# Performance work log

Measured on AMD Instinct MI355X. Metric: run time of the kernel, lower is better.

Reference implementation:

```python
import jax, jax.numpy as jnp
import numpy as np

B, R, N, DN, DR, H, Q, NB = 32, 10, 512, 128, 128, 128, 256, 16


def setup_inputs() -> dict:
    key = jax.random.key(0)
    ks = jax.random.split(key, 14)
    inp = {
        'node_features': jax.random.normal(ks[0], (B, N, DN), jnp.float32),
        'relation_features': jax.random.normal(ks[1], (B, R, DR), jnp.float32),
        'adj': jax.random.uniform(ks[2], (B, R, N, N), jnp.float32),
        'obs': jax.random.normal(ks[3], (B, Q, H), jnp.float32),
        'node_mask': jnp.ones((B, N), jnp.float32),
        'obs_mask': jnp.ones((B, Q), jnp.float32),
        # RGCN params (single layer: hidden_dims=[128])
        'Wb': jax.random.normal(ks[4], (NB, (DN + DR) * R), jnp.float32) * 0.02,  # bottleneck (no bias)
        'Ww': jax.random.normal(ks[5], (H, NB), jnp.float32) * 0.1,               # weight (no bias)
        'rgcn_bias': jnp.zeros((), jnp.float32),                                   # scalar bias (filled 0)
        # ContextQueryAttention params
        'w_C': jax.random.normal(ks[6], (H,), jnp.float32) * 0.05,
        'w_Q': jax.random.normal(ks[7], (H,), jnp.float32) * 0.05,
        'w_CQ': jax.random.normal(ks[8], (H,), jnp.float32) * 0.05,
        'cq_bias': jnp.zeros((), jnp.float32),
        # ReprAggregator output linear (shared for both directions)
        'lin_W': jax.random.normal(ks[9], (H, 4 * H), jnp.float32) * 0.02,
        'lin_b': jnp.zeros((H,), jnp.float32),
    }
    return inp


def _masked_softmax(s, mask, axis):
    return jax.nn.softmax(jnp.where(mask > 0, s, -jnp.inf), axis=axis)


def _rgcn(node_features, relation_features, adj, Wb, Ww, rgcn_bias):
    b, n = node_features.shape[0], node_features.shape[1]
    # per-relation concat: (B,R,N,DN+DR)
    nf = jnp.broadcast_to(node_features[:, None], (b, R, n, node_features.shape[-1]))
    rf = jnp.broadcast_to(relation_features[:, :, None, :], (b, R, n, relation_features.shape[-1]))
    cat = jnp.concatenate([nf, rf], axis=-1)
    # per-relation bmm, gathered in relation order along feature dim: (B,N,R*(DN+DR))
    sup = jnp.einsum('brnm,brmd->bnrd', adj, cat)
    sup = sup.reshape(b, n, R * cat.shape[-1])
    h = sup @ Wb.T            # (B,N,NB)
    h = h @ Ww.T              # (B,N,H)
    return jax.nn.sigmoid(h + rgcn_bias)


def _cqattn(ctx, query, ctx_mask, query_mask, w_C, w_Q, w_CQ, cq_bias):
    # trilinear similarity: (B,Lc,Lq)
    res_C = ctx @ w_C                                  # (B,Lc)
    res_Q = query @ w_Q                                # (B,Lq)
    res_CQ = jnp.einsum('bch,bqh->bcq', ctx * w_CQ, query)
    S = res_C[:, :, None] + res_Q[:, None, :] + res_CQ + cq_bias
    s_ctx = _masked_softmax(S, ctx_mask[:, :, None], axis=1)     # softmax over ctx dim
    s_query = _masked_softmax(S, query_mask[:, None, :], axis=2)  # softmax over query dim
    P = jnp.einsum('bcq,bqh->bch', s_query, query)
    Qm = jnp.einsum('bcq,bdq,bdh->bch', s_query, s_ctx, ctx)
    return jnp.concatenate([ctx, P, ctx * P, ctx * Qm], axis=-1)  # (B,Lc,4H)


def reference(node_features, relation_features, adj, obs, node_mask, obs_mask,
              Wb, Ww, rgcn_bias, w_C, w_Q, w_CQ, cq_bias, lin_W, lin_b):
    # GraphEncoder (single RGCN layer)
    node_repr = _rgcn(node_features, relation_features, adj, Wb, Ww, rgcn_bias)
    # ReprAggregator between obs text repr and node repr
    a1 = _cqattn(obs, node_repr, obs_mask, node_mask, w_C, w_Q, w_CQ, cq_bias)
    a2 = _cqattn(node_repr, obs, node_mask, obs_mask, w_C, w_Q, w_CQ, cq_bias)
    h_og = a1 @ lin_W.T + lin_b   # (B,Q,H)
    h_go = a2 @ lin_W.T + lin_b   # (B,N,H)
    return h_og, h_go
```

## Files before the change

### kernel.cpp

```cpp
#include <hip/hip_runtime.h>
#include <hip/hip_bf16.h>
#include <stdint.h>

typedef unsigned short u16;
typedef __attribute__((ext_vector_type(8))) short short8;
typedef __attribute__((ext_vector_type(4))) float f32x4;

#define DEVI static __device__ __forceinline__

constexpr int B = 32, R = 10, N = 512, H = 128, Q = 256, NB = 16;
constexpr int KWB = 2560;

DEVI u16 f2u(float f) { return __builtin_bit_cast(unsigned short, __float2bfloat16(f)); }
DEVI float u2f(u16 u) { union { uint32_t i; float f; } c; c.i = ((uint32_t)u) << 16; return c.f; }

DEVI float wredmax(float v) { for (int o = 32; o; o >>= 1) v = fmaxf(v, __shfl_xor(v, o)); return v; }
DEVI float wredsum(float v) { for (int o = 32; o; o >>= 1) v += __shfl_xor(v, o); return v; }

DEVI short8 cvt8(const float* p) {
  float4 f0 = *(const float4*)p;
  float4 f1 = *(const float4*)(p + 4);
  short8 v;
  v[0] = (short)f2u(f0.x); v[1] = (short)f2u(f0.y);
  v[2] = (short)f2u(f0.z); v[3] = (short)f2u(f0.w);
  v[4] = (short)f2u(f1.x); v[5] = (short)f2u(f1.y);
  v[6] = (short)f2u(f1.z); v[7] = (short)f2u(f1.w);
  return v;
}

__global__ __launch_bounds__(256) void k_prep(
    const float* __restrict__ linW, u16* __restrict__ linWb,
    const float* __restrict__ Wb, u16* __restrict__ WbB,
    const float* __restrict__ Ww, u16* __restrict__ WwB,
    const float* __restrict__ rf, float* __restrict__ vv,
    const float* __restrict__ obs, const float* __restrict__ wC,
    const float* __restrict__ wQ, const float* __restrict__ wCQ,
    u16* __restrict__ obsW, float* __restrict__ a_o, float* __restrict__ d_o,
    u16* __restrict__ obsT) {
  int bid = blockIdx.x, t = threadIdx.x;
  __shared__ float sa[4], sd[4];
  __shared__ u16 tile[32][33];
  if (bid < 64) {
    int i = bid * 256 + t;
    float4 f = ((const float4*)linW)[i];
    ushort4 o;
    o.x = f2u(f.x); o.y = f2u(f.y); o.z = f2u(f.z); o.w = f2u(f.w);
    ((ushort4*)linWb)[i] = o;
  } else if (bid < 144) {
    int rk = (bid - 64) * 2 + (t >> 7);
    int d = t & 127;
    int r = rk / NB, k = rk % NB;
    WbB[(long)rk * 128 + d] = f2u(Wb[(long)k * KWB + r * 256 + d]);
  } else if (bid < 160) {
    int idx = (bid - 144) * 256 + t;
    int h = idx >> 5, kb = idx & 31;
    WwB[idx] = (kb < NB) ? f2u(Ww[h * NB + kb]) : (u16)0;
  } else if (bid < 1440) {
    int w = t >> 6, lane = t & 63;
    int gid = (bid - 160) * 4 + w;
    int b = gid / (R * NB), rk = gid % (R * NB), r = rk / NB, k = rk % NB;
    float s = 0.f;
    for (int dd = 0; dd < 2; ++dd) {
      int d = lane + dd * 64;
      s += rf[((long)b * R + r) * H + d] * Wb[(long)k * KWB + r * 256 + 128 + d];
    }
    s = wredsum(s);
    if (lane == 0) vv[((long)b * R + r) * NB + k] = s;
  } else if (bid < 5536) {
    int row = (bid - 1440) * 2 + (t >> 7);
    int tt = t & 127;
    float x = obs[(long)row * H + tt];
    obsW[(long)row * H + tt] = f2u(x * wCQ[tt]);
    float aa = wredsum(x * wC[tt]);
    float dd2 = wredsum(x * wQ[tt]);
    int wv = t >> 6;
    if ((t & 63) == 0) { sa[wv] = aa; sd[wv] = dd2; }
    __syncthreads();
    if ((t & 127) == 0) {
      int h = t >> 7;
      a_o[row] = sa[h * 2] + sa[h * 2 + 1];
      d_o[row] = sd[h * 2] + sd[h * 2 + 1];
    }
  } else {
    int id = bid - 5536;
    int cx = id & 3, ry = (id >> 2) & 7, b = id >> 5;
    int c0 = cx * 32, r0 = ry * 32;
    int tx = t & 31, ty = t >> 5;
    for (int i = 0; i < 4; i++) {
      int r = r0 + ty + i * 8, c = c0 + tx;
      tile[ty + i * 8][tx] = f2u(obs[((long)b * Q + r) * H + c]);
    }
    __syncthreads();
    for (int i = 0; i < 4; i++) {
      int c = c0 + ty + i * 8, r = r0 + tx;
      obsT[((long)b * H + c) * Q + r] = tile[tx][ty + i * 8];
    }
  }
}

__global__ __launch_bounds__(512) void k_tt(const u16* __restrict__ WbB, const float* __restrict__ nf,
                                            const float* __restrict__ vv, u16* __restrict__ tT) {
  int bx = blockIdx.x, b = blockIdx.y;
  int t = threadIdx.x;
  __shared__ __align__(16) u16 tile[128][128];
  {
    int row = t >> 2, q = (t & 3) * 32;
    const float* src = nf + ((long)b * N + bx * 128 + row) * H + q;
    int sw = (row & 7) << 3;
    for (int j = 0; j < 4; j++) {
      short8 v = cvt8(src + j * 8);
      *(short8*)&tile[row][(q + j * 8) ^ sw] = v;
    }
  }
  __syncthreads();
  int w = t >> 6, lane = t & 63;
  int rw = lane & 15, kq = lane >> 4;
  for (int r = w; r < R; r += 8) {
    f32x4 acc[8] = {};
    for (int kit = 0; kit < H; kit += 32) {
      short8 av = *(const short8*)(WbB + ((long)r * NB + rw) * 128 + kit + kq * 8);
#pragma unroll
      for (int nt = 0; nt < 8; nt++) {
        int brow = nt * 16 + rw;
        short8 bv = *(const short8*)&tile[brow][(kit + kq * 8) ^ ((brow & 7) << 3)];
        acc[nt] = __builtin_amdgcn_mfma_f32_16x16x32_bf16(av, bv, acc[nt], 0, 0, 0);
      }
    }
    long rbase = (long)(b * R + r) * NB;
#pragma unroll
    for (int nt = 0; nt < 8; nt++) {
      int gc = bx * 128 + nt * 16 + rw;
      for (int i = 0; i < 4; i++) {
        int gr = kq * 4 + i;
        tT[(rbase + gr) * N + gc] = f2u(acc[nt][i] + vv[rbase + gr]);
      }
    }
  }
}

__global__ __launch_bounds__(512) void k_rgcn(
    const float* __restrict__ adj, const u16* __restrict__ tT,
    const u16* __restrict__ WwB, const float* __restrict__ rb,
    const float* __restrict__ wC, const float* __restrict__ wQ,
    u16* __restrict__ nr, u16* __restrict__ nrT,
    float* __restrict__ b_n, float* __restrict__ c_n) {
  int ntile = blockIdx.x, b = blockIdx.y;
  int n0 = ntile * 16;
  int tid = threadIdx.x;
  int w = tid >> 6, lane = tid & 63;
  int rw = lane & 15, kq = lane >> 4;
  __shared__ float hred[8][16][17];
  __shared__ __align__(16) u16 hbf[16][32];
  __shared__ float bpc[8][16][2];
  float rbv = rb[0];

  f32x4 acc = {0.f, 0.f, 0.f, 0.f};
#pragma unroll 4
  for (int j = 0; j < 20; ++j) {
    int kkk = w + 8 * j;
    int r = kkk >> 4, k = (kkk & 15) * 32;
    short8 av = cvt8(adj + (((long)(b * R + r) * N) + n0 + rw) * N + k + kq * 8);
    short8 bv = *(const short8*)(tT + ((long)(b * R + r) * NB + rw) * N + k + kq * 8);
    acc = __builtin_amdgcn_mfma_f32_16x16x32_bf16(av, bv, acc, 0, 0, 0);
  }
  for (int i = 0; i < 4; i++) hred[w][kq * 4 + i][rw] = acc[i];
  __syncthreads();
  if (tid < 256) {
    int n = tid >> 4, kb = tid & 15;
    float s = 0.f;
    for (int ww = 0; ww < 8; ww++) s += hred[ww][n][kb];
    hbf[n][kb] = f2u(s);
    hbf[n][kb + 16] = 0;
  }
  __syncthreads();

  short8 av = *(const short8*)&hbf[rw][kq * 8];
  short8 bv = *(const short8*)(WwB + (long)(w * 16 + rw) * 32 + kq * 8);
  f32x4 a2 = {0.f, 0.f, 0.f, 0.f};
  a2 = __builtin_amdgcn_mfma_f32_16x16x32_bf16(av, bv, a2, 0, 0, 0);
  int h = w * 16 + rw;
  float wq = wQ[h], wc = wC[h];
  float bsum[4], csum[4];
  for (int i = 0; i < 4; i++) {
    float s = 1.f / (1.f + expf(-(a2[i] + rbv)));
    int n = n0 + kq * 4 + i;
    u16 sv = f2u(s);
    nr[((long)b * N + n) * H + h] = sv;
    nrT[((long)b * H + h) * N + n] = sv;
    bsum[i] = s * wq;
    csum[i] = s * wc;
  }
  for (int i = 0; i < 4; i++) {
    for (int o = 8; o; o >>= 1) { bsum[i] += __shfl_xor(bsum[i], o); csum[i] += __shfl_xor(csum[i], o); }
  }
  if (rw == 0)
    for (int i = 0; i < 4; i++) { bpc[w][kq * 4 + i][0] = bsum[i]; bpc[w][kq * 4 + i][1] = csum[i]; }
  __syncthreads();
  if (tid < 32) {
    int ns = tid & 15, which = tid >> 4;
    float s = 0.f;
    for (int ww = 0; ww < 8; ww++) s += bpc[ww][ns][which];
    (which ? c_n : b_n)[(long)b * N + n0 + ns] = s;
  }
}

__global__ __launch_bounds__(512) void k_mm_soft(
    const u16* __restrict__ obsW, const u16* __restrict__ nr,
    const float* __restrict__ b_n, const float* __restrict__ c_n,
    const float* __restrict__ nmask,
    u16* __restrict__ sq1, u16* __restrict__ sc2, u16* __restrict__ ST) {
  int mt = blockIdx.x, b = blockIdx.y;
  int tid = threadIdx.x;
  int w = tid >> 6, lane = tid & 63;
  int rw = lane & 15, kq = lane >> 4;
  __shared__ float sm1[8][16], sm2[8][16], ss1[8][16], ss2[8][16];

  const u16* ap = obsW + ((long)b * Q + mt * 16 + rw) * H + kq * 8;
  const u16* bp = nr + ((long)b * N + w * 64 + rw) * H + kq * 8;
  f32x4 acc[4] = {};
  for (int k = 0; k < H; k += 32) {
    short8 av = *(const short8*)(ap + k);
#pragma unroll
    for (int nt = 0; nt < 4; nt++) {
      short8 bv = *(const short8*)(bp + (long)nt * 16 * H + k);
      acc[nt] = __builtin_amdgcn_mfma_f32_16x16x32_bf16(av, bv, acc[nt], 0, 0, 0);
    }
  }
  float bn[4], cn[4];
  bool mk[4];
  int gcv[4];
#pragma unroll
  for (int nt = 0; nt < 4; nt++) {
    int gc = w * 64 + nt * 16 + rw;
    gcv[nt] = gc;
    mk[nt] = nmask[(long)b * N + gc] > 0.f;
    bn[nt] = b_n[(long)b * N + gc];
    cn[nt] = c_n[(long)b * N + gc];
  }
#pragma unroll
  for (int nt = 0; nt < 4; nt++) {
    long stb = ((long)b * N + gcv[nt]) * Q + mt * 16 + kq * 4;
    for (int i = 0; i < 4; i++) ST[stb + i] = f2u(acc[nt][i]);
  }
  float m1[4], m2[4];
  for (int i = 0; i < 4; i++) { m1[i] = -1e30f; m2[i] = -1e30f; }
#pragma unroll
  for (int nt = 0; nt < 4; nt++)
    for (int i = 0; i < 4; i++) {
      float s = acc[nt][i];
      if (mk[nt]) { m1[i] = fmaxf(m1[i], s + bn[nt]); m2[i] = fmaxf(m2[i], s + cn[nt]); }
    }
  for (int i = 0; i < 4; i++)
    for (int o = 8; o; o >>= 1) { m1[i] = fmaxf(m1[i], __shfl_xor(m1[i], o)); m2[i] = fmaxf(m2[i], __shfl_xor(m2[i], o)); }
  if (rw == 0)
    for (int i = 0; i < 4; i++) { sm1[w][kq * 4 + i] = m1[i]; sm2[w][kq * 4 + i] = m2[i]; }
  __syncthreads();
  for (int i = 0; i < 4; i++) {
    float g1 = -1e30f, g2 = -1e30f;
    for (int ww = 0; ww < 8; ww++) { g1 = fmaxf(g1, sm1[ww][kq * 4 + i]); g2 = fmaxf(g2, sm2[ww][kq * 4 + i]); }
    m1[i] = g1; m2[i] = g2;
  }
  float e1[4][4], e2[4][4];
  float s1[4] = {0.f, 0.f, 0.f, 0.f}, s2[4] = {0.f, 0.f, 0.f, 0.f};
#pragma unroll
  for (int nt = 0; nt < 4; nt++)
    for (int i = 0; i < 4; i++) {
      float s = acc[nt][i];
      float a = mk[nt] ? expf(s + bn[nt] - m1[i]) : 0.f;
      float c = mk[nt] ? expf(s + cn[nt] - m2[i]) : 0.f;
      e1[nt][i] = a; e2[nt][i] = c;
      s1[i] += a; s2[i] += c;
    }
  for (int i = 0; i < 4; i++)
    for (int o = 8; o; o >>= 1) { s1[i] += __shfl_xor(s1[i], o); s2[i] += __shfl_xor(s2[i], o); }
  if (rw == 0)
    for (int i = 0; i < 4; i++) { ss1[w][kq * 4 + i] = s1[i]; ss2[w][kq * 4 + i] = s2[i]; }
  __syncthreads();
  float r1[4], r2[4];
  for (int i = 0; i < 4; i++) {
    float g1 = 0.f, g2 = 0.f;
    for (int ww = 0; ww < 8; ww++) { g1 += ss1[ww][kq * 4 + i]; g2 += ss2[ww][kq * 4 + i]; }
    r1[i] = 1.f / g1; r2[i] = 1.f / g2;
  }
#pragma unroll
  for (int nt = 0; nt < 4; nt++)
    for (int i = 0; i < 4; i++) {
      long ob = ((long)b * Q + mt * 16 + kq * 4 + i) * N + gcv[nt];
      sq1[ob] = f2u(e1[nt][i] * r1[i]);
      sc2[ob] = f2u(e2[nt][i] * r2[i]);
    }
}

__global__ __launch_bounds__(256) void k_soft_col(
    const u16* __restrict__ ST, const float* __restrict__ a_o, const float* __restrict__ d_o,
    const float* __restrict__ omask, u16* __restrict__ sc1T, u16* __restrict__ sq2) {
  int id = blockIdx.x;
  int b = id / N;
  int o = threadIdx.x;
  long rn = id;
  __shared__ float s1a[4], s2a[4];
  float mv = u2f(ST[rn * Q + o]);
  bool on = omask[(long)b * Q + o] > 0.f;
  float v1 = on ? a_o[(long)b * Q + o] + mv : -1e30f;
  float v2 = on ? d_o[(long)b * Q + o] + mv : -1e30f;
  float m1 = wredmax(v1), m2 = wredmax(v2);
  int wv = o >> 6;
  if ((o & 63) == 0) { s1a[wv] = m1; s2a[wv] = m2; }
  __syncthreads();
  m1 = fmaxf(fmaxf(s1a[0], s1a[1]), fmaxf(s1a[2], s1a[3]));
  m2 = fmaxf(fmaxf(s2a[0], s2a[1]), fmaxf(s2a[2], s2a[3]));
  __syncthreads();
  float e1 = expf(v1 - m1), e2 = expf(v2 - m2);
  float s1 = wredsum(e1), s2 = wredsum(e2);
  if ((o & 63) == 0) { s1a[wv] = s1; s2a[wv] = s2; }
  __syncthreads();
  float r1 = 1.f / (s1a[0] + s1a[1] + s1a[2] + s1a[3]);
  float r2 = 1.f / (s2a[0] + s2a[1] + s2a[2] + s2a[3]);
  sc1T[rn * Q + o] = f2u(e1 * r1);
  sq2[rn * Q + o] = f2u(e2 * r2);
}

struct GPar {
  const u16* A; const u16* Bt; u16* C;
  int Mdim; int Kdim; long sA, sBt, sC; int tc;
};
__global__ __launch_bounds__(64) void gemm_quad8(GPar p0, GPar p1, GPar p2, GPar p3) {
  int z = blockIdx.z;
  GPar p = (z == 0) ? p0 : (z == 1) ? p1 : (z == 2) ? p2 : p3;
  int mt = blockIdx.x;
  if (mt * 16 >= p.Mdim) return;
  int batch = blockIdx.y;
  int lane = threadIdx.x;
  int rw = lane & 15, kq = lane >> 4;
  const u16* ap = p.A + (long)batch * p.sA + (long)(mt * 16 + rw) * p.Kdim + kq * 8;
  const u16* bp = p.Bt + (long)batch * p.sBt + (long)rw * p.Kdim + kq * 8;
  f32x4 acc[8] = {};
  for (int k = 0; k < p.Kdim; k += 32) {
    short8 av = *(const short8*)(ap + k);
#pragma unroll
    for (int nt = 0; nt < 8; nt++) {
      short8 bv = *(const short8*)(bp + (long)nt * 16 * p.Kdim + k);
      acc[nt] = __builtin_amdgcn_mfma_f32_16x16x32_bf16(av, bv, acc[nt], 0, 0, 0);
    }
  }
#pragma unroll
  for (int nt = 0; nt < 8; nt++) {
    int gc = nt * 16 + rw;
    for (int i = 0; i < 4; i++) {
      int gr = mt * 16 + kq * 4 + i;
      long idx = p.tc ? ((long)gc * p.Mdim + gr) : ((long)gr * H + gc);
      p.C[(long)batch * p.sC + idx] = f2u(acc[nt][i]);
    }
  }
}

__global__ __launch_bounds__(64) void gemm_cat2(
    const float* __restrict__ obs, const u16* __restrict__ nrr,
    const u16* __restrict__ P1, const u16* __restrict__ Qm1,
    const u16* __restrict__ P2, const u16* __restrict__ Qm2,
    const u16* __restrict__ Wt, const float* __restrict__ bias,
    float* __restrict__ out0, float* __restrict__ out1) {
  int z = blockIdx.z;
  int Mdim = z ? N : Q;
  int mt = blockIdx.x;
  if (mt * 16 >= Mdim) return;
  int batch = blockIdx.y;
  const u16* P = z ? P2 : P1;
  const u16* Qm = z ? Qm2 : Qm1;
  float* out = z ? out1 : out0;
  int lane = threadIdx.x;
  int rw = lane & 15, kq = lane >> 4;
  long arow = (long)batch * Mdim + mt * 16 + rw;
  const u16* bp = Wt + (long)rw * (4 * H) + kq * 8;
  f32x4 acc[8] = {};
  for (int k = 0; k < 4 * H; k += 32) {
    int sec = k >> 7;
    int off = (k & 127) + kq * 8;
    long rb2 = arow * H + off;
    short8 av;
    if (sec == 0) {
      if (!z) av = cvt8(obs + rb2);
      else    av = *(const short8*)(nrr + rb2);
    } else if (sec == 1) {
      av = *(const short8*)(P + rb2);
    } else {
      float xf[8];
      if (!z) {
        const float* xp = obs + rb2;
        float4 f0 = *(const float4*)xp;
        float4 f1 = *(const float4*)(xp + 4);
        xf[0] = f0.x; xf[1] = f0.y; xf[2] = f0.z; xf[3] = f0.w;
        xf[4] = f1.x; xf[5] = f1.y; xf[6] = f1.z; xf[7] = f1.w;
      } else {
        short8 xv = *(const short8*)(nrr + rb2);
        for (int i = 0; i < 8; i++) xf[i] = u2f((u16)xv[i]);
      }
      short8 pv = *(const short8*)((sec == 2 ? P : Qm) + rb2);
      for (int i = 0; i < 8; i++) av[i] = (short)f2u(xf[i] * u2f((u16)pv[i]));
    }
#pragma unroll
    for (int nt = 0; nt < 8; nt++) {
      short8 bv = *(const short8*)(bp + (long)nt * 16 * (4 * H) + k);
      acc[nt] = __builtin_amdgcn_mfma_f32_16x16x32_bf16(av, bv, acc[nt], 0, 0, 0);
    }
  }
#pragma unroll
  for (int nt = 0; nt < 8; nt++) {
    int gc = nt * 16 + rw;
    float cb = bias[gc];
    for (int i = 0; i < 4; i++) {
      int gr = mt * 16 + kq * 4 + i;
      out[((long)batch * Mdim + gr) * H + gc] = acc[nt][i] + cb;
    }
  }
}

extern "C" void kernel_launch(void* const* d_in, const int* in_sizes, int n_in,
                              void* d_out, int out_size, void* d_ws, size_t ws_size,
                              hipStream_t stream) {
  const float* nf    = (const float*)d_in[0];
  const float* rf    = (const float*)d_in[1];
  const float* adj   = (const float*)d_in[2];
  const float* obs   = (const float*)d_in[3];
  const float* nmask = (const float*)d_in[4];
  const float* omask = (const float*)d_in[5];
  const float* Wb    = (const float*)d_in[6];
  const float* Ww    = (const float*)d_in[7];
  const float* rb    = (const float*)d_in[8];
  const float* wC    = (const float*)d_in[9];
  const float* wQ    = (const float*)d_in[10];
  const float* wCQ   = (const float*)d_in[11];
  const float* linW  = (const float*)d_in[13];
  const float* linb  = (const float*)d_in[14];
  float* outp = (float*)d_out;

  char* w = (char*)d_ws;
  auto alloc = [&](size_t bytes) { char* p = w; w += (bytes + 255) & ~(size_t)255; return p; };
  u16*   linWb = (u16*)  alloc((size_t)H * 4 * H * 2);
  u16*   WbB   = (u16*)  alloc((size_t)R * NB * 128 * 2);
  u16*   WwB   = (u16*)  alloc((size_t)H * 32 * 2);
  float* vv    = (float*)alloc((size_t)B * R * NB * 4);
  u16*   obsW  = (u16*)  alloc((size_t)B * Q * H * 2);
  u16*   obsT  = (u16*)  alloc((size_t)B * H * Q * 2);
  float* a_o   = (float*)alloc((size_t)B * Q * 4);
  float* d_o   = (float*)alloc((size_t)B * Q * 4);
  float* b_n   = (float*)alloc((size_t)B * N * 4);
  float* c_n   = (float*)alloc((size_t)B * N * 4);
  u16*   nr    = (u16*)  alloc((size_t)B * N * H * 2);
  u16*   nrT   = (u16*)  alloc((size_t)B * H * N * 2);
  u16*   tT    = (u16*)  alloc((size_t)B * R * NB * N * 2);
  u16*   ST    = (u16*)  alloc((size_t)B * N * Q * 2);
  u16*   sq1   = (u16*)  alloc((size_t)B * Q * N * 2);
  u16*   sc2   = (u16*)  alloc((size_t)B * Q * N * 2);
  u16*   sc1T  = (u16*)  alloc((size_t)B * N * Q * 2);
  u16*   sq2   = (u16*)  alloc((size_t)B * N * Q * 2);
  u16*   P1    = (u16*)  alloc((size_t)B * Q * H * 2);
  u16*   T1T   = (u16*)  alloc((size_t)B * H * N * 2);
  u16*   Qm1   = (u16*)  alloc((size_t)B * Q * H * 2);
  u16*   P2    = (u16*)  alloc((size_t)B * N * H * 2);
  u16*   T2T   = (u16*)  alloc((size_t)B * H * Q * 2);
  u16*   Qm2   = (u16*)  alloc((size_t)B * N * H * 2);

  k_prep<<<6560, 256, 0, stream>>>(linW, linWb, Wb, WbB, Ww, WwB,
                                   rf, vv, obs, wC, wQ, wCQ, obsW, a_o, d_o, obsT);
  k_tt<<<dim3(N / 128, B), 512, 0, stream>>>(WbB, nf, vv, tT);
  k_rgcn<<<dim3(N / 16, B), 512, 0, stream>>>(adj, tT, WwB, rb, wC, wQ, nr, nrT, b_n, c_n);
  k_mm_soft<<<dim3(Q / 16, B), 512, 0, stream>>>(obsW, nr, b_n, c_n, nmask, sq1, sc2, ST);
  k_soft_col<<<B * N, 256, 0, stream>>>(ST, a_o, d_o, omask, sc1T, sq2);
  GPar pP1  = {sq1,  nrT,  P1,  Q, N, (long)Q * N, (long)H * N, (long)Q * H, 0};
  GPar pT2T = {sc2,  nrT,  T2T, Q, N, (long)Q * N, (long)H * N, (long)H * Q, 1};
  GPar pT1T = {sc1T, obsT, T1T, N, Q, (long)N * Q, (long)H * Q, (long)H * N, 1};
  GPar pP2  = {sq2,  obsT, P2,  N, Q, (long)N * Q, (long)H * Q, (long)N * H, 0};
  gemm_quad8<<<dim3(N / 16, B, 4), 64, 0, stream>>>(pP1, pT2T, pT1T, pP2);
  GPar pQm1 = {sq1, T1T, Qm1, Q, N, (long)Q * N, (long)H * N, (long)Q * H, 0};
  GPar pQm2 = {sq2, T2T, Qm2, N, Q, (long)N * Q, (long)H * Q, (long)N * H, 0};
  gemm_quad8<<<dim3(N / 16, B, 2), 64, 0, stream>>>(pQm1, pQm2, pQm1, pQm2);
  gemm_cat2<<<dim3(N / 16, B, 2), 64, 0, stream>>>(obs, nr, P1, Qm1, P2, Qm2,
                                                   linWb, linb, outp, outp + (long)B * Q * H);

  (void)in_sizes; (void)n_in; (void)out_size; (void)ws_size;
}
```

Before: 282.4 us.

## Remap block indices for XCD locality and use wave-per-row column softmax

Adds a block-index permutation to k_tt, k_rgcn, k_mm_soft and the GEMM kernels. Consecutive hardware block IDs are spread round-robin over the 8 XCDs, so the remap gives each XCD a contiguous range of batches/tiles, meant to improve L2 reuse of shared operands. The column softmax kernel now handles one row per wave with 4 elements per lane, which removes the shared-memory reductions and __syncthreads and cuts the block count by four. The GEMM launches are flattened to 1D grids with explicit kernels instead of a struct-dispatch kernel. The remap assumes an 8-XCD round-robin dispatch order.

```diff
diff --git a/kernel.cpp b/kernel.cpp
--- a/kernel.cpp
+++ b/kernel.cpp
@@ -100,7 +100,9 @@
 
 __global__ __launch_bounds__(512) void k_tt(const u16* __restrict__ WbB, const float* __restrict__ nf,
                                             const float* __restrict__ vv, u16* __restrict__ tT) {
-  int bx = blockIdx.x, b = blockIdx.y;
+  int f = blockIdx.x + 4 * blockIdx.y;
+  int g = (f & 7) * 16 + (f >> 3);
+  int bx = g & 3, b = g >> 2;
   int t = threadIdx.x;
   __shared__ __align__(16) u16 tile[128][128];
   {
@@ -144,7 +146,9 @@
     const float* __restrict__ wC, const float* __restrict__ wQ,
     u16* __restrict__ nr, u16* __restrict__ nrT,
     float* __restrict__ b_n, float* __restrict__ c_n) {
-  int ntile = blockIdx.x, b = blockIdx.y;
+  int f = blockIdx.x + 32 * blockIdx.y;
+  int g = (f & 7) * 128 + (f >> 3);
+  int ntile = g & 31, b = g >> 5;
   int n0 = ntile * 16;
   int tid = threadIdx.x;
   int w = tid >> 6, lane = tid & 63;
@@ -209,7 +213,9 @@
     const float* __restrict__ b_n, const float* __restrict__ c_n,
     const float* __restrict__ nmask,
     u16* __restrict__ sq1, u16* __restrict__ sc2, u16* __restrict__ ST) {
-  int mt = blockIdx.x, b = blockIdx.y;
+  int f = blockIdx.x + 16 * blockIdx.y;
+  int g = (f & 7) * 64 + (f >> 3);
+  int mt = g & 15, b = g >> 4;
   int tid = threadIdx.x;
   int w = tid >> 6, lane = tid & 63;
   int rw = lane & 15, kq = lane >> 4;
@@ -294,52 +300,45 @@
 __global__ __launch_bounds__(256) void k_soft_col(
     const u16* __restrict__ ST, const float* __restrict__ a_o, const float* __restrict__ d_o,
     const float* __restrict__ omask, u16* __restrict__ sc1T, u16* __restrict__ sq2) {
-  int id = blockIdx.x;
-  int b = id / N;
-  int o = threadIdx.x;
-  long rn = id;
-  __shared__ float s1a[4], s2a[4];
-  float mv = u2f(ST[rn * Q + o]);
-  bool on = omask[(long)b * Q + o] > 0.f;
-  float v1 = on ? a_o[(long)b * Q + o] + mv : -1e30f;
-  float v2 = on ? d_o[(long)b * Q + o] + mv : -1e30f;
-  float m1 = wredmax(v1), m2 = wredmax(v2);
-  int wv = o >> 6;
-  if ((o & 63) == 0) { s1a[wv] = m1; s2a[wv] = m2; }
-  __syncthreads();
-  m1 = fmaxf(fmaxf(s1a[0], s1a[1]), fmaxf(s1a[2], s1a[3]));
-  m2 = fmaxf(fmaxf(s2a[0], s2a[1]), fmaxf(s2a[2], s2a[3]));
-  __syncthreads();
-  float e1 = expf(v1 - m1), e2 = expf(v2 - m2);
-  float s1 = wredsum(e1), s2 = wredsum(e2);
-  if ((o & 63) == 0) { s1a[wv] = s1; s2a[wv] = s2; }
-  __syncthreads();
-  float r1 = 1.f / (s1a[0] + s1a[1] + s1a[2] + s1a[3]);
-  float r2 = 1.f / (s2a[0] + s2a[1] + s2a[2] + s2a[3]);
-  sc1T[rn * Q + o] = f2u(e1 * r1);
-  sq2[rn * Q + o] = f2u(e2 * r2);
-}
-
-struct GPar {
-  const u16* A; const u16* Bt; u16* C;
-  int Mdim; int Kdim; long sA, sBt, sC; int tc;
-};
-__global__ __launch_bounds__(64) void gemm_quad8(GPar p0, GPar p1, GPar p2, GPar p3) {
-  int z = blockIdx.z;
-  GPar p = (z == 0) ? p0 : (z == 1) ? p1 : (z == 2) ? p2 : p3;
-  int mt = blockIdx.x;
-  if (mt * 16 >= p.Mdim) return;
-  int batch = blockIdx.y;
-  int lane = threadIdx.x;
+  int w = threadIdx.x >> 6, lane = threadIdx.x & 63;
+  long rn = (long)blockIdx.x * 4 + w;
+  int b = (int)(rn >> 9);
+  float v1[4], v2[4];
+  const u16* st = ST + rn * Q + lane * 4;
+  for (int i = 0; i < 4; i++) {
+    int o = lane * 4 + i;
+    float mv = u2f(st[i]);
+    bool on = omask[(long)b * Q + o] > 0.f;
+    v1[i] = on ? a_o[(long)b * Q + o] + mv : -1e30f;
+    v2[i] = on ? d_o[(long)b * Q + o] + mv : -1e30f;
+  }
+  float m1 = wredmax(fmaxf(fmaxf(v1[0], v1[1]), fmaxf(v1[2], v1[3])));
+  float m2 = wredmax(fmaxf(fmaxf(v2[0], v2[1]), fmaxf(v2[2], v2[3])));
+  float e1[4], e2[4], s1 = 0.f, s2 = 0.f;
+  for (int i = 0; i < 4; i++) {
+    e1[i] = expf(v1[i] - m1); e2[i] = expf(v2[i] - m2);
+    s1 += e1[i]; s2 += e2[i];
+  }
+  s1 = wredsum(s1); s2 = wredsum(s2);
+  float r1 = 1.f / s1, r2 = 1.f / s2;
+  for (int i = 0; i < 4; i++) {
+    sc1T[rn * Q + lane * 4 + i] = f2u(e1[i] * r1);
+    sq2[rn * Q + lane * 4 + i] = f2u(e2[i] * r2);
+  }
+}
+
+DEVI void gemm_tile(const u16* A, const u16* Bt, u16* C, int Mdim, int Kdim,
+                    long sA, long sBt, long sC, int tc, int batch, int mt, int lane) {
+  if (mt * 16 >= Mdim) return;
   int rw = lane & 15, kq = lane >> 4;
-  const u16* ap = p.A + (long)batch * p.sA + (long)(mt * 16 + rw) * p.Kdim + kq * 8;
-  const u16* bp = p.Bt + (long)batch * p.sBt + (long)rw * p.Kdim + kq * 8;
+  const u16* ap = A + (long)batch * sA + (long)(mt * 16 + rw) * Kdim + kq * 8;
+  const u16* bp = Bt + (long)batch * sBt + (long)rw * Kdim + kq * 8;
   f32x4 acc[8] = {};
-  for (int k = 0; k < p.Kdim; k += 32) {
+  for (int k = 0; k < Kdim; k += 32) {
     short8 av = *(const short8*)(ap + k);
 #pragma unroll
     for (int nt = 0; nt < 8; nt++) {
-      short8 bv = *(const short8*)(bp + (long)nt * 16 * p.Kdim + k);
+      short8 bv = *(const short8*)(bp + (long)nt * 16 * Kdim + k);
       acc[nt] = __builtin_amdgcn_mfma_f32_16x16x32_bf16(av, bv, acc[nt], 0, 0, 0);
     }
   }
@@ -348,23 +347,50 @@
     int gc = nt * 16 + rw;
     for (int i = 0; i < 4; i++) {
       int gr = mt * 16 + kq * 4 + i;
-      long idx = p.tc ? ((long)gc * p.Mdim + gr) : ((long)gr * H + gc);
-      p.C[(long)batch * p.sC + idx] = f2u(acc[nt][i]);
-    }
-  }
-}
-
-__global__ __launch_bounds__(64) void gemm_cat2(
+      long idx = tc ? ((long)gc * Mdim + gr) : ((long)gr * H + gc);
+      C[(long)batch * sC + idx] = f2u(acc[nt][i]);
+    }
+  }
+}
+
+__global__ __launch_bounds__(64) void k_gemmA(
+    const u16* __restrict__ sq1, const u16* __restrict__ sc2,
+    const u16* __restrict__ sc1T, const u16* __restrict__ sq2,
+    const u16* __restrict__ nrT, const u16* __restrict__ obsT,
+    u16* __restrict__ P1, u16* __restrict__ T2T, u16* __restrict__ T1T, u16* __restrict__ P2) {
+  int bid = blockIdx.x;
+  int t = (bid & 7) * 512 + (bid >> 3);
+  int z = t >> 10, rem = t & 1023, batch = rem >> 5, mt = rem & 31;
+  int lane = threadIdx.x;
+  if (z == 0)      gemm_tile(sq1,  nrT,  P1,  Q, N, (long)Q * N, (long)H * N, (long)Q * H, 0, batch, mt, lane);
+  else if (z == 1) gemm_tile(sc2,  nrT,  T2T, Q, N, (long)Q * N, (long)H * N, (long)H * Q, 1, batch, mt, lane);
+  else if (z == 2) gemm_tile(sc1T, obsT, T1T, N, Q, (long)N * Q, (long)H * Q, (long)H * N, 1, batch, mt, lane);
+  else             gemm_tile(sq2,  obsT, P2,  N, Q, (long)N * Q, (long)H * Q, (long)N * H, 0, batch, mt, lane);
+}
+
+__global__ __launch_bounds__(64) void k_gemmB(
+    const u16* __restrict__ sq1, const u16* __restrict__ sq2,
+    const u16* __restrict__ T1T, const u16* __restrict__ T2T,
+    u16* __restrict__ Qm1, u16* __restrict__ Qm2) {
+  int bid = blockIdx.x;
+  int t = (bid & 7) * 256 + (bid >> 3);
+  int z = t >> 10, rem = t & 1023, batch = rem >> 5, mt = rem & 31;
+  int lane = threadIdx.x;
+  if (z == 0) gemm_tile(sq1, T1T, Qm1, Q, N, (long)Q * N, (long)H * N, (long)Q * H, 0, batch, mt, lane);
+  else        gemm_tile(sq2, T2T, Qm2, N, Q, (long)N * Q, (long)H * Q, (long)N * H, 0, batch, mt, lane);
+}
+
+__global__ __launch_bounds__(64) void k_cat(
     const float* __restrict__ obs, const u16* __restrict__ nrr,
     const u16* __restrict__ P1, const u16* __restrict__ Qm1,
     const u16* __restrict__ P2, const u16* __restrict__ Qm2,
     const u16* __restrict__ Wt, const float* __restrict__ bias,
     float* __restrict__ out0, float* __restrict__ out1) {
-  int z = blockIdx.z;
+  int bid = blockIdx.x;
+  int t = (bid & 7) * 256 + (bid >> 3);
+  int z = t >> 10, rem = t & 1023, batch = rem >> 5, mt = rem & 31;
   int Mdim = z ? N : Q;
-  int mt = blockIdx.x;
   if (mt * 16 >= Mdim) return;
-  int batch = blockIdx.y;
   const u16* P = z ? P2 : P1;
   const u16* Qm = z ? Qm2 : Qm1;
   float* out = z ? out1 : out0;
@@ -460,23 +486,17 @@
   u16*   P2    = (u16*)  alloc((size_t)B * N * H * 2);
   u16*   T2T   = (u16*)  alloc((size_t)B * H * Q * 2);
   u16*   Qm2   = (u16*)  alloc((size_t)B * N * H * 2);
+  float* out1  = outp + (long)B * Q * H;
 
   k_prep<<<6560, 256, 0, stream>>>(linW, linWb, Wb, WbB, Ww, WwB,
                                    rf, vv, obs, wC, wQ, wCQ, obsW, a_o, d_o, obsT);
   k_tt<<<dim3(N / 128, B), 512, 0, stream>>>(WbB, nf, vv, tT);
   k_rgcn<<<dim3(N / 16, B), 512, 0, stream>>>(adj, tT, WwB, rb, wC, wQ, nr, nrT, b_n, c_n);
   k_mm_soft<<<dim3(Q / 16, B), 512, 0, stream>>>(obsW, nr, b_n, c_n, nmask, sq1, sc2, ST);
-  k_soft_col<<<B * N, 256, 0, stream>>>(ST, a_o, d_o, omask, sc1T, sq2);
-  GPar pP1  = {sq1,  nrT,  P1,  Q, N, (long)Q * N, (long)H * N, (long)Q * H, 0};
-  GPar pT2T = {sc2,  nrT,  T2T, Q, N, (long)Q * N, (long)H * N, (long)H * Q, 1};
-  GPar pT1T = {sc1T, obsT, T1T, N, Q, (long)N * Q, (long)H * Q, (long)H * N, 1};
-  GPar pP2  = {sq2,  obsT, P2,  N, Q, (long)N * Q, (long)H * Q, (long)N * H, 0};
-  gemm_quad8<<<dim3(N / 16, B, 4), 64, 0, stream>>>(pP1, pT2T, pT1T, pP2);
-  GPar pQm1 = {sq1, T1T, Qm1, Q, N, (long)Q * N, (long)H * N, (long)Q * H, 0};
-  GPar pQm2 = {sq2, T2T, Qm2, N, Q, (long)N * Q, (long)H * Q, (long)N * H, 0};
-  gemm_quad8<<<dim3(N / 16, B, 2), 64, 0, stream>>>(pQm1, pQm2, pQm1, pQm2);
-  gemm_cat2<<<dim3(N / 16, B, 2), 64, 0, stream>>>(obs, nr, P1, Qm1, P2, Qm2,
-                                                   linWb, linb, outp, outp + (long)B * Q * H);
+  k_soft_col<<<B * N / 4, 256, 0, stream>>>(ST, a_o, d_o, omask, sc1T, sq2);
+  k_gemmA<<<4096, 64, 0, stream>>>(sq1, sc2, sc1T, sq2, nrT, obsT, P1, T2T, T1T, P2);
+  k_gemmB<<<2048, 64, 0, stream>>>(sq1, sq2, T1T, T2T, Qm1, Qm2);
+  k_cat<<<2048, 64, 0, stream>>>(obs, nr, P1, Qm1, P2, Qm2, linWb, linb, outp, out1);
 
   (void)in_sizes; (void)n_in; (void)out_size; (void)ws_size;
 }
```

Result: no change. 284.8 us (+0.9%).
